# Kernel optimization log

Hardware: AMD Instinct MI355X
Metric: run time of the kernel (lower is better)

## Reference

```python
import jax, jax.numpy as jnp
import numpy as np

N = 2_000_000
D = 128
S = 100_000


def setup_inputs() -> dict:
    key = jax.random.key(0)
    k1, k2, k3 = jax.random.split(key, 3)
    # small scale keeps exp(logit) well within fp32 range
    features = jax.random.normal(k1, (N, D), dtype=jnp.float32) * 0.05
    w = jax.random.normal(k2, (D,), dtype=jnp.float32) * 0.05
    phrase_id = jax.random.randint(k3, (N,), 0, S)
    unique_phrase = jnp.arange(S)
    return {"features": features, "w": w, "phrase_id": phrase_id,
            "unique_phrase": unique_phrase}


def reference(features, w, phrase_id, unique_phrase):
    # logit_i = exp(gamma(features)_i), gamma is a bias-free Linear(D, 1)
    logit = jnp.exp(features @ w)                               # [N]
    # per-segment partition function via scatter-add, then gather back
    partition = jax.ops.segment_sum(logit, phrase_id,
                                    num_segments=unique_phrase.shape[0])  # [S]
    weights = logit / partition[phrase_id]                      # [N]
    return weights[:, None]                                     # [N, 1]
```

## Files before the change

### kernel.cpp

```cpp
#include <hip/hip_runtime.h>


__global__ void logit_partition_kernel(const float4* __restrict__ F4,
                                       const float* __restrict__ w,
                                       const int* __restrict__ pid,
                                       float* __restrict__ logit,
                                       float* __restrict__ part,
                                       int nrows) {
    const int lane = threadIdx.x & 63;
    const int l32  = lane & 31;
    const int half = lane >> 5;
    const int wave  = (blockIdx.x * blockDim.x + threadIdx.x) >> 6;
    const int nwave = (gridDim.x * blockDim.x) >> 6;

    const float4 wf = reinterpret_cast<const float4*>(w)[l32];

    const int ntile = nrows / 16;
    const int nmain = ntile * 16;

    for (int t = wave; t < ntile; t += nwave) {
        const int r = t * 16;

        float4 f[8];
        #pragma unroll
        for (int j = 0; j < 8; ++j)
            f[j] = F4[(size_t)(r + 2 * j + half) * 32 + l32];

        float s[8];
        #pragma unroll
        for (int j = 0; j < 8; ++j)
            s[j] = f[j].x * wf.x + f[j].y * wf.y + f[j].z * wf.z + f[j].w * wf.w;

        float m[4];
        #pragma unroll
        for (int j = 0; j < 4; ++j) {
            float u = s[2*j]   + __shfl_xor(s[2*j],   16, 64);
            float v = s[2*j+1] + __shfl_xor(s[2*j+1], 16, 64);
            m[j] = (l32 & 16) ? v : u;
        }
        float n[2];
        #pragma unroll
        for (int j = 0; j < 2; ++j) {
            float u = m[2*j]   + __shfl_xor(m[2*j],   8, 64);
            float v = m[2*j+1] + __shfl_xor(m[2*j+1], 8, 64);
            n[j] = (l32 & 8) ? v : u;
        }
        float u = n[0] + __shfl_xor(n[0], 4, 64);
        float v = n[1] + __shfl_xor(n[1], 4, 64);
        float tt = (l32 & 4) ? v : u;
        tt += __shfl_xor(tt, 2, 64);
        tt += __shfl_xor(tt, 1, 64);

        if ((l32 & 3) == 0) {
            const int jidx = ((l32 >> 2) & 1) * 4 + ((l32 >> 3) & 1) * 2 +
                             ((l32 >> 4) & 1);
            const int row = r + 2 * jidx + half;
            float lg = expf(tt);
            logit[row] = lg;
            atomicAdd(&part[pid[row]], lg);
        }
    }

    for (int r = nmain + wave * 2; r < nrows; r += nwave * 2) {
        const int row = r + half;
        if (row < nrows) {
            float4 f = F4[(size_t)row * 32 + l32];
            float s = f.x * wf.x + f.y * wf.y + f.z * wf.z + f.w * wf.w;
            #pragma unroll
            for (int o = 16; o; o >>= 1) s += __shfl_xor(s, o, 64);
            if (l32 == 0) {
                float lg = expf(s);
                logit[row] = lg;
                atomicAdd(&part[pid[row]], lg);
            }
        }
    }
}

__global__ void weights_kernel(const float4* __restrict__ logit4,
                               const int4* __restrict__ pid4,
                               const float* __restrict__ part,
                               float4* __restrict__ out4,
                               int nvec,
                               const float* __restrict__ logit,
                               const int* __restrict__ pid,
                               float* __restrict__ out,
                               int n) {
    int i = blockIdx.x * blockDim.x + threadIdx.x;
    const int stride = gridDim.x * blockDim.x;
    for (; i < nvec; i += stride) {
        float4 lg = logit4[i];
        int4 p = pid4[i];
        float4 o;
        o.x = lg.x / part[p.x];
        o.y = lg.y / part[p.y];
        o.z = lg.z / part[p.z];
        o.w = lg.w / part[p.w];
        out4[i] = o;
    }
    if (blockIdx.x == 0 && threadIdx.x == 0) {
        for (int j = nvec * 4; j < n; ++j) out[j] = logit[j] / part[pid[j]];
    }
}

extern "C" void kernel_launch(void* const* d_in, const int* in_sizes, int n_in,
                              void* d_out, int out_size, void* d_ws, size_t ws_size,
                              hipStream_t stream) {
    const float* features = (const float*)d_in[0];
    const float* w        = (const float*)d_in[1];
    const int*   pid      = (const int*)d_in[2];

    const int N = in_sizes[2];
    const int S = in_sizes[3];

    float* logit = (float*)d_ws;
    float* part  = logit + N;
    float* out   = (float*)d_out;

    hipMemsetAsync(part, 0, (size_t)S * sizeof(float), stream);

    logit_partition_kernel<<<dim3(2048), dim3(256), 0, stream>>>(
        (const float4*)features, w, pid, logit, part, N);

    {
        const int nvec = N / 4;
        int blocks = (nvec + 255) / 256;
        if (blocks > 2048) blocks = 2048;
        weights_kernel<<<dim3(blocks), dim3(256), 0, stream>>>(
            (const float4*)logit, (const int4*)pid, part, (float4*)out, nvec,
            logit, pid, out, N);
    }
}
```

Measured before the change: 229.8 us.

## Split atomic segment-sum out of logit kernel and use nontemporal feature loads

The fused logit/partition kernel is split in two. The first kernel now only streams the feature matrix with nontemporal loads and writes exp logits. A separate kernel then reads logits and phrase ids as vectors and does the scatter-add atomics. The aim is to keep the bandwidth-bound feature stream from stalling on scattered atomics and to avoid polluting the cache with the features. The cost is an extra launch and an extra pass over the logits and ids.

```diff
diff --git a/kernel.cpp b/kernel.cpp
--- a/kernel.cpp
+++ b/kernel.cpp
@@ -1,19 +1,19 @@
 #include <hip/hip_runtime.h>
 
 
-__global__ void logit_partition_kernel(const float4* __restrict__ F4,
-                                       const float* __restrict__ w,
-                                       const int* __restrict__ pid,
-                                       float* __restrict__ logit,
-                                       float* __restrict__ part,
-                                       int nrows) {
+typedef float f32x4 __attribute__((ext_vector_type(4)));
+
+__global__ void logit_kernel(const f32x4* __restrict__ F4,
+                             const float* __restrict__ w,
+                             float* __restrict__ logit,
+                             int nrows) {
     const int lane = threadIdx.x & 63;
     const int l32  = lane & 31;
     const int half = lane >> 5;
     const int wave  = (blockIdx.x * blockDim.x + threadIdx.x) >> 6;
     const int nwave = (gridDim.x * blockDim.x) >> 6;
 
-    const float4 wf = reinterpret_cast<const float4*>(w)[l32];
+    const f32x4 wf = reinterpret_cast<const f32x4*>(w)[l32];
 
     const int ntile = nrows / 16;
     const int nmain = ntile * 16;
@@ -21,10 +21,11 @@
     for (int t = wave; t < ntile; t += nwave) {
         const int r = t * 16;
 
-        float4 f[8];
+        f32x4 f[8];
         #pragma unroll
         for (int j = 0; j < 8; ++j)
-            f[j] = F4[(size_t)(r + 2 * j + half) * 32 + l32];
+            f[j] = __builtin_nontemporal_load(
+                &F4[(size_t)(r + 2 * j + half) * 32 + l32]);
 
         float s[8];
         #pragma unroll
@@ -55,25 +56,41 @@
             const int jidx = ((l32 >> 2) & 1) * 4 + ((l32 >> 3) & 1) * 2 +
                              ((l32 >> 4) & 1);
             const int row = r + 2 * jidx + half;
-            float lg = expf(tt);
-            logit[row] = lg;
-            atomicAdd(&part[pid[row]], lg);
+            logit[row] = expf(tt);
         }
     }
 
     for (int r = nmain + wave * 2; r < nrows; r += nwave * 2) {
         const int row = r + half;
         if (row < nrows) {
-            float4 f = F4[(size_t)row * 32 + l32];
+            f32x4 f = F4[(size_t)row * 32 + l32];
             float s = f.x * wf.x + f.y * wf.y + f.z * wf.z + f.w * wf.w;
             #pragma unroll
             for (int o = 16; o; o >>= 1) s += __shfl_xor(s, o, 64);
-            if (l32 == 0) {
-                float lg = expf(s);
-                logit[row] = lg;
-                atomicAdd(&part[pid[row]], lg);
-            }
+            if (l32 == 0) logit[row] = expf(s);
         }
+    }
+}
+
+__global__ void segsum_kernel(const float4* __restrict__ logit4,
+                              const int4* __restrict__ pid4,
+                              float* __restrict__ part,
+                              int nvec,
+                              const float* __restrict__ logit,
+                              const int* __restrict__ pid,
+                              int n) {
+    int i = blockIdx.x * blockDim.x + threadIdx.x;
+    const int stride = gridDim.x * blockDim.x;
+    for (; i < nvec; i += stride) {
+        float4 lg = logit4[i];
+        int4 p = pid4[i];
+        atomicAdd(&part[p.x], lg.x);
+        atomicAdd(&part[p.y], lg.y);
+        atomicAdd(&part[p.z], lg.z);
+        atomicAdd(&part[p.w], lg.w);
+    }
+    if (blockIdx.x == 0 && threadIdx.x == 0) {
+        for (int j = nvec * 4; j < n; ++j) atomicAdd(&part[pid[j]], logit[j]);
     }
 }
 
@@ -117,17 +134,19 @@
     float* part  = logit + N;
     float* out   = (float*)d_out;
 
-    hipMemsetAsync(part, 0, (size_t)S * sizeof(float), stream);
+    (void)hipMemsetAsync(part, 0, (size_t)S * sizeof(float), stream);
 
-    logit_partition_kernel<<<dim3(2048), dim3(256), 0, stream>>>(
-        (const float4*)features, w, pid, logit, part, N);
+    logit_kernel<<<dim3(2048), dim3(256), 0, stream>>>(
+        (const f32x4*)features, w, logit, N);
 
-    {
-        const int nvec = N / 4;
-        int blocks = (nvec + 255) / 256;
-        if (blocks > 2048) blocks = 2048;
-        weights_kernel<<<dim3(blocks), dim3(256), 0, stream>>>(
-            (const float4*)logit, (const int4*)pid, part, (float4*)out, nvec,
-            logit, pid, out, N);
-    }
+    const int nvec = N / 4;
+    int blocks = (nvec + 255) / 256;
+    if (blocks > 2048) blocks = 2048;
+
+    segsum_kernel<<<dim3(blocks), dim3(256), 0, stream>>>(
+        (const float4*)logit, (const int4*)pid, part, nvec, logit, pid, N);
+
+    weights_kernel<<<dim3(blocks), dim3(256), 0, stream>>>(
+        (const float4*)logit, (const int4*)pid, part, (float4*)out, nvec,
+        logit, pid, out, N);
 }
```

After: 286.0 us. 1.24x slower.
